# Performance work log

Measured on AMD Instinct MI355X. Metric: run time of the kernel, lower is better.

## Reference

```python
import jax, jax.numpy as jnp
import numpy as np

B, N, D, O, H, R = 32, 1024, 1024, 1024, 512, 64
TOPK = 4
MAX_GAIN = 0.1
SCALE = 1.0
LN_EPS = 1e-5


def _dct_basis(dim, num_bases):
    pos = np.arange(dim, dtype=np.float64)[None, :]
    modes = np.arange(num_bases, dtype=np.float64)[:, None]
    basis = np.cos(np.pi / dim * (pos + 0.5) * modes)
    basis[0] = basis[0] / np.sqrt(2.0)
    basis = basis * np.sqrt(2.0 / dim)
    return jnp.asarray(basis, jnp.float32)


def setup_inputs() -> dict:
    key = jax.random.key(0)
    ks = jax.random.split(key, 16)
    s = 0.02
    return {
        'x': jax.random.normal(ks[0], (B, N, D), jnp.float32),
        'context': jax.random.normal(ks[1], (B, H), jnp.float32),
        'input_basis': _dct_basis(D, R),                       # [R, D] (buffer)
        'output_basis': s * jax.random.normal(ks[2], (R, O), jnp.float32),
        'ln_gamma': jnp.ones((D,), jnp.float32),
        'ln_beta': jnp.zeros((D,), jnp.float32),
        'w1': s * jax.random.normal(ks[3], (D, H), jnp.float32),
        'b1': jnp.zeros((H,), jnp.float32),
        'w2': s * jax.random.normal(ks[4], (H, H), jnp.float32),
        'b2': jnp.zeros((H,), jnp.float32),
        'wg': s * jax.random.normal(ks[5], (H, R * R), jnp.float32),
        'bg': jnp.zeros((R * R,), jnp.float32),
        'wl': s * jax.random.normal(ks[6], (H, R * R), jnp.float32),
        'bl': jnp.zeros((R * R,), jnp.float32),
        'wm': s * jax.random.normal(ks[7], (2 * H, R), jnp.float32),
        'bm': 1.5 * jnp.ones((R,), jnp.float32),
        'wgain': s * jax.random.normal(ks[8], (2 * H, R), jnp.float32),
        'bgain': jnp.zeros((R,), jnp.float32),
        'wgate': s * jax.random.normal(ks[9], (2 * H, 1), jnp.float32),
        'bgate': -1.0 * jnp.ones((1,), jnp.float32),
        'wa': s * jax.random.normal(ks[10], (2 * H, 1), jnp.float32),
        'ba': -1.0 * jnp.ones((1,), jnp.float32),
        'wb': s * jax.random.normal(ks[11], (2 * H, 1), jnp.float32),
        'bb': jnp.zeros((1,), jnp.float32),
    }


def _detail_summary(x, topk):
    # x: [B, N, D] with token 0 = CLS; pick topk highest-variance patch tokens
    pt = x[:, 1:]                                   # [B, N-1, D]
    pm = jnp.mean(pt, axis=1, keepdims=True)
    scores = jnp.mean((pt - pm) ** 2, axis=-1)      # [B, N-1]
    _, idx = jax.lax.top_k(scores, topk)            # [B, k]
    gathered = jnp.take_along_axis(pt, idx[:, :, None], axis=1)  # [B, k, D]
    return jnp.mean(gathered, axis=1)               # [B, D]


def _skew(a):
    return 0.5 * (a - jnp.swapaxes(a, -1, -2))


def reference(x, context, input_basis, output_basis, ln_gamma, ln_beta,
              w1, b1, w2, b2, wg, bg, wl, bl, wm, bm,
              wgain, bgain, wgate, bgate, wa, ba, wb, bb):
    b = x.shape[0]
    r = input_basis.shape[0]

    detail = _detail_summary(x, TOPK)               # [B, D]
    mu = jnp.mean(detail, axis=-1, keepdims=True)
    var = jnp.var(detail, axis=-1, keepdims=True)
    h = (detail - mu) * jax.lax.rsqrt(var + LN_EPS) * ln_gamma + ln_beta
    h = jax.nn.gelu(h @ w1 + b1, approximate=False)
    local_context = h @ w2 + b2                     # [B, H]
    fused = jnp.concatenate([context, local_context], axis=-1)  # [B, 2H]

    global_skew = _skew((context @ wg + bg).reshape(b, r, r))
    local_skew = _skew((local_context @ wl + bl).reshape(b, r, r))
    mode_mask = jax.nn.sigmoid(fused @ wm + bm)     # [B, R]
    # diag(m) @ A @ diag(m) == m_i * A_ij * m_j
    mg = mode_mask[:, :, None] * global_skew * mode_mask[:, None, :]
    ml = mode_mask[:, :, None] * local_skew * mode_mask[:, None, :]
    comm = ml @ mg - mg @ ml                        # [B, R, R]

    alpha = SCALE * 0.5 * jax.nn.sigmoid(fused @ wa + ba)   # [B, 1]
    beta = SCALE * 0.25 * jnp.tanh(fused @ wb + bb)         # [B, 1]
    omega = alpha[:, :, None] * 0.5 * (mg + ml) + beta[:, :, None] * (comm / 12.0)

    q = jax.vmap(jax.scipy.linalg.expm)(omega)              # [B, R, R]
    gains = 1.0 + MAX_GAIN * jnp.tanh(fused @ wgain + bgain)  # [B, R]
    operator = q * gains[:, None, :]                        # q @ diag(gains)

    proj = jnp.einsum('bnd,rd->bnr', x, input_basis)        # [B, N, R]
    gate = SCALE * jax.nn.sigmoid(fused @ wgate + bgate)    # [B, 1]
    transformed = jnp.einsum('bnr,brk->bnk', proj, operator)
    delta = gate[:, None, :] * (transformed - proj)         # [B, N, R]
    out = jnp.einsum('bnr,ro->bno', delta, output_basis)    # [B, N, O]
    return out
```

## Files before the change

### kernel.cpp

```cpp
#include <hip/hip_runtime.h>
#include <math.h>

#define NB 32
#define NN 1024
#define ND 1024
#define NO 1024
#define NH 512
#define NR 64

#define OFF_PM     0u
#define OFF_PMSQ   32768u
#define OFF_ROWSQ  32800u
#define OFF_G      65568u
#define OFF_H0     98336u
#define OFF_H1     131104u
#define OFF_LOCAL  147488u
#define OFF_P1     163872u
#define OFF_P2     294944u
#define OFF_PG     360480u
#define OFF_PL     884768u
#define OFF_AG     1409056u
#define OFF_AL     1540128u
#define OFF_MASK   1671200u
#define OFF_GAINS  1673248u
#define OFF_SCAL   1675296u
#define OFF_MFIN   1675424u
#define OFF_C      1806496u
#define OFF_PROJ   3903648u

__global__ __launch_bounds__(256) void k0_colsum(const float* __restrict__ x, float* __restrict__ part){
  int tid = threadIdx.x;
  int nseg = blockIdx.x, b = blockIdx.y;
  int d4 = tid*4;
  const float* xp = x + (size_t)b*NN*ND + d4;
  int nstart = nseg*64; if(nseg==0) nstart = 1;
  int nend = nseg*64 + 64;
  float sx=0.f, sy=0.f, sz=0.f, sw=0.f;
  #pragma unroll 4
  for(int n=nstart; n<nend; n++){
    float4 v = *(const float4*)&xp[(size_t)n*ND];
    sx+=v.x; sy+=v.y; sz+=v.z; sw+=v.w;
  }
  *(float4*)&part[(size_t)(b*16+nseg)*1024 + d4] = make_float4(sx,sy,sz,sw);
}

__global__ __launch_bounds__(256) void k1_pmreduce(const float* __restrict__ part, float* __restrict__ pm, float* __restrict__ pmsq){
  __shared__ float red[256];
  int b = blockIdx.x, tid = threadIdx.x;
  float acc = 0.f;
  #pragma unroll
  for(int i=0;i<4;i++){
    int d = i*256 + tid;
    float s = 0.f;
    #pragma unroll
    for(int ks=0;ks<16;ks++) s += part[(size_t)(b*16+ks)*1024 + d];
    float p = s * (1.0f/1023.0f);
    pm[b*1024+d] = p;
    acc += p*p;
  }
  red[tid] = acc; __syncthreads();
  for(int o=128;o>0;o>>=1){ if(tid<o) red[tid]+=red[tid+o]; __syncthreads(); }
  if(tid==0) pmsq[b] = red[0]*(1.0f/1024.0f);
}

__global__ __launch_bounds__(256) void k2_proj(const float* __restrict__ x, const float* __restrict__ basis,
    const float* __restrict__ pm, float* __restrict__ proj, float* __restrict__ rowsq, float* __restrict__ G){
  __shared__ __align__(16) float xs[64][68];
  __shared__ __align__(16) float bs[64][68];
  int tid = threadIdx.x;
  int row0 = blockIdx.x*64;
  int b = row0 >> 10;
  int lrow = tid>>4, lkv = tid&15;
  int rg = tid>>4, cg = tid&15;
  float acc[4][4];
  #pragma unroll
  for(int i_=0;i_<4;i_++){ acc[i_][0]=0.f; acc[i_][1]=0.f; acc[i_][2]=0.f; acc[i_][3]=0.f; }
  float sq[4]={0.f,0.f,0.f,0.f}, gp[4]={0.f,0.f,0.f,0.f};
  for(int kc=0;kc<16;kc++){
    int k0 = kc*64;
    float4 p4 = *(const float4*)&pm[(size_t)b*ND + k0 + lkv*4];
    #pragma unroll
    for(int i=0;i<4;i++){
      int r = lrow + 16*i;
      float4 v = *(const float4*)&x[((size_t)(row0+r))*ND + k0 + lkv*4];
      xs[lkv*4+0][r]=v.x; xs[lkv*4+1][r]=v.y; xs[lkv*4+2][r]=v.z; xs[lkv*4+3][r]=v.w;
      sq[i] += v.x*v.x + v.y*v.y + v.z*v.z + v.w*v.w;
      gp[i] += v.x*p4.x + v.y*p4.y + v.z*p4.z + v.w*p4.w;
      float4 u = *(const float4*)&basis[((size_t)r)*ND + k0 + lkv*4];
      bs[lkv*4+0][r]=u.x; bs[lkv*4+1][r]=u.y; bs[lkv*4+2][r]=u.z; bs[lkv*4+3][r]=u.w;
    }
    __syncthreads();
    #pragma unroll 8
    for(int kk=0;kk<64;kk++){
      float4 a = *(const float4*)&xs[kk][rg*4];
      float4 bb= *(const float4*)&bs[kk][cg*4];
      float ar[4]={a.x,a.y,a.z,a.w};
      float br[4]={bb.x,bb.y,bb.z,bb.w};
      #pragma unroll
      for(int i_=0;i_<4;i_++){
        #pragma unroll
        for(int j_=0;j_<4;j_++) acc[i_][j_] += ar[i_]*br[j_];
      }
    }
    __syncthreads();
  }
  #pragma unroll
  for(int i_=0;i_<4;i_++){
    float4 v = make_float4(acc[i_][0],acc[i_][1],acc[i_][2],acc[i_][3]);
    *(float4*)&proj[((size_t)(row0 + rg*4 + i_))*NR + cg*4] = v;
  }
  __syncthreads();
  #pragma unroll
  for(int i=0;i<4;i++){ int r = lrow+16*i; xs[r][lkv]=sq[i]; bs[r][lkv]=gp[i]; }
  __syncthreads();
  if(tid<64){
    float s=0.f, g=0.f;
    #pragma unroll
    for(int c=0;c<16;c++){ s+=xs[tid][c]; g+=bs[tid][c]; }
    rowsq[row0+tid]=s; G[row0+tid]=g;
  }
}

__global__ __launch_bounds__(256) void k3_detail(const float* __restrict__ x, const float* __restrict__ rowsq,
    const float* __restrict__ G, const float* __restrict__ pmsq,
    const float* __restrict__ gamma_, const float* __restrict__ beta_, float* __restrict__ h0){
  __shared__ float sc[1024];
  __shared__ float rv[256];
  __shared__ int ri[256];
  __shared__ int topi[4];
  __shared__ float mred[256];
  int b = blockIdx.x, tid = threadIdx.x;
  float ps = pmsq[b];
  const float invD = 1.0f/1024.0f;
  for(int n=tid;n<1024;n+=256)
    sc[n] = (n==0) ? -INFINITY : (rowsq[b*1024+n] - 2.0f*G[b*1024+n])*invD + ps;
  __syncthreads();
  for(int t=0;t<4;t++){
    float bv = -INFINITY; int bi = 0x7fffffff;
    for(int n=tid;n<1024;n+=256){
      float v = sc[n];
      if(v>bv || (v==bv && n<bi)){ bv=v; bi=n; }
    }
    rv[tid]=bv; ri[tid]=bi;
    __syncthreads();
    for(int o=128;o>0;o>>=1){
      if(tid<o){
        float v=rv[tid+o]; int ii=ri[tid+o];
        if(v>rv[tid] || (v==rv[tid] && ii<ri[tid])){ rv[tid]=v; ri[tid]=ii; }
      }
      __syncthreads();
    }
    if(tid==0){ topi[t]=ri[0]; sc[ri[0]] = -INFINITY; }
    __syncthreads();
  }
  int i0=topi[0], i1=topi[1], i2=topi[2], i3=topi[3];
  float dv[4]; float dsum=0.f;
  #pragma unroll
  for(int jj=0;jj<4;jj++){
    int d = tid + jj*256;
    float v = 0.25f*(x[((size_t)(b*NN+i0))*ND+d] + x[((size_t)(b*NN+i1))*ND+d]
                   + x[((size_t)(b*NN+i2))*ND+d] + x[((size_t)(b*NN+i3))*ND+d]);
    dv[jj]=v; dsum+=v;
  }
  mred[tid]=dsum; __syncthreads();
  for(int o=128;o>0;o>>=1){ if(tid<o) mred[tid]+=mred[tid+o]; __syncthreads(); }
  float mu = mred[0]*invD;
  __syncthreads();
  float vs=0.f;
  #pragma unroll
  for(int jj=0;jj<4;jj++){ float t2=dv[jj]-mu; vs+=t2*t2; }
  mred[tid]=vs; __syncthreads();
  for(int o=128;o>0;o>>=1){ if(tid<o) mred[tid]+=mred[tid+o]; __syncthreads(); }
  float var = mred[0]*invD;
  float rstd = rsqrtf(var + 1e-5f);
  #pragma unroll
  for(int jj=0;jj<4;jj++){
    int d = tid + jj*256;
    h0[b*1024+d] = (dv[jj]-mu)*rstd*gamma_[d] + beta_[d];
  }
}

__global__ __launch_bounds__(256) void gemm32_partial(const float* __restrict__ V, const float* __restrict__ W,
      float* __restrict__ part, int Kd, int Ncols){
  __shared__ __align__(16) float Vs[128][36];
  int col = blockIdx.x*256 + threadIdx.x;
  int k0 = blockIdx.y*128;
  for(int i=threadIdx.x; i<4096; i+=256){ int r=i>>7, k=i&127; Vs[k][r] = V[(size_t)r*Kd + k0 + k]; }
  __syncthreads();
  float acc[32];
  #pragma unroll
  for(int r=0;r<32;r++) acc[r]=0.f;
  #pragma unroll 4
  for(int k=0;k<128;k++){
    float wv = W[(size_t)(k0+k)*Ncols + col];
    #pragma unroll
    for(int r4=0;r4<8;r4++){
      float4 v = *(const float4*)&Vs[k][r4*4];
      acc[r4*4+0]+=v.x*wv; acc[r4*4+1]+=v.y*wv; acc[r4*4+2]+=v.z*wv; acc[r4*4+3]+=v.w*wv;
    }
  }
  #pragma unroll
  for(int r=0;r<32;r++) part[((size_t)(blockIdx.y*32 + r))*Ncols + col] = acc[r];
}

__global__ __launch_bounds__(256) void k_red_gelu(const float* __restrict__ part, const float* __restrict__ b1, float* __restrict__ h1){
  int id = blockIdx.x*256 + threadIdx.x;
  int b_ = id >> 9, j = id & 511;
  float s = b1[j];
  #pragma unroll
  for(int ks=0;ks<8;ks++) s += part[(size_t)(ks*32+b_)*512 + j];
  h1[id] = 0.5f*s*(1.0f + erff(s*0.70710678118654752440f));
}
__global__ __launch_bounds__(256) void k_red_local(const float* __restrict__ part, const float* __restrict__ b2, float* __restrict__ lcl){
  int id = blockIdx.x*256 + threadIdx.x;
  int b_ = id >> 9, j = id & 511;
  float s = b2[j];
  #pragma unroll
  for(int ks=0;ks<4;ks++) s += part[(size_t)(ks*32+b_)*512 + j];
  lcl[id] = s;
}
__global__ __launch_bounds__(256) void k_red_gl(const float* __restrict__ pg, const float* __restrict__ pl,
    const float* __restrict__ bg, const float* __restrict__ bl, float* __restrict__ Ag, float* __restrict__ Al){
  int id = blockIdx.x*256 + threadIdx.x;
  int c = id & 4095;
  int b_ = id >> 12;
  float sg = bg[c], sl = bl[c];
  #pragma unroll
  for(int ks=0;ks<4;ks++){
    sg += pg[(size_t)(ks*32 + b_)*4096 + c];
    sl += pl[(size_t)(ks*32 + b_)*4096 + c];
  }
  Ag[id] = sg; Al[id] = sl;
}

__global__ __launch_bounds__(1024) void k_heads(const float* __restrict__ context, const float* __restrict__ lcl,
    const float* __restrict__ wm, const float* __restrict__ bm,
    const float* __restrict__ wgain, const float* __restrict__ bgain,
    const float* __restrict__ wgate, const float* __restrict__ bgate,
    const float* __restrict__ wa, const float* __restrict__ ba,
    const float* __restrict__ wb, const float* __restrict__ bb,
    float* __restrict__ mask, float* __restrict__ gains, float* __restrict__ scal){
  __shared__ float fs[1024];
  __shared__ float redm[16][64];
  __shared__ float redg[16][64];
  __shared__ float wra[16], wrb[16], wrg[16];
  int b = blockIdx.x, tid = threadIdx.x;
  fs[tid] = (tid < 512) ? context[b*512 + tid] : lcl[b*512 + tid - 512];
  __syncthreads();
  int j = tid & 63, kq = tid >> 6;
  const float* wmp = wm    + (size_t)(kq*64)*64 + j;
  const float* wgp = wgain + (size_t)(kq*64)*64 + j;
  float am = 0.f, ag = 0.f;
  #pragma unroll 8
  for(int k=0;k<64;k++){
    float f = fs[kq*64 + k];
    am += f * wmp[k*64];
    ag += f * wgp[k*64];
  }
  redm[kq][j] = am; redg[kq][j] = ag;
  float f = fs[tid];
  float pa = f*wa[tid], pb = f*wb[tid], pg = f*wgate[tid];
  #pragma unroll
  for(int o=32;o>0;o>>=1){
    pa += __shfl_down(pa, o);
    pb += __shfl_down(pb, o);
    pg += __shfl_down(pg, o);
  }
  if(j == 0){ wra[kq]=pa; wrb[kq]=pb; wrg[kq]=pg; }
  __syncthreads();
  for(int o=8;o>0;o>>=1){
    if(kq < o){ redm[kq][j] += redm[kq+o][j]; redg[kq][j] += redg[kq+o][j]; }
    __syncthreads();
  }
  if(tid < 64){
    float m = redm[0][tid] + bm[tid];
    mask[b*64+tid] = 1.0f/(1.0f+expf(-m));
    float g = redg[0][tid] + bgain[tid];
    gains[b*64+tid] = 1.0f + 0.1f*tanhf(g);
  }
  if(tid == 0){
    float sa=0.f, sb=0.f, sg=0.f;
    #pragma unroll
    for(int i=0;i<16;i++){ sa+=wra[i]; sb+=wrb[i]; sg+=wrg[i]; }
    scal[b*4+0] = 0.5f/(1.0f+expf(-(sa+ba[0])));
    scal[b*4+1] = 0.25f*tanhf(sb+bb[0]);
    scal[b*4+2] = 1.0f/(1.0f+expf(-(sg+bgate[0])));
  }
}

__global__ __launch_bounds__(1024) void k7_expm(const float* __restrict__ Ag, const float* __restrict__ Al,
    const float* __restrict__ mask, const float* __restrict__ gains, const float* __restrict__ scal,
    float* __restrict__ Mfin){
  __shared__ __align__(16) float B0s[64][66];
  __shared__ __align__(16) float B1s[64][66];
  __shared__ __align__(16) float B2s[64][66];
  __shared__ float msks[64];
  __shared__ float colsum[64];
  __shared__ int ssh;
  int b = blockIdx.x, tid = threadIdx.x;
  int ig = tid>>5, jg = tid&31;
  int i0 = ig*2, j0 = jg*2;
  if(tid<64) msks[tid] = mask[b*64+tid];
  __syncthreads();
  float alpha = scal[b*4+0], bta = scal[b*4+1], gate = scal[b*4+2];
  const float* ag = Ag + b*4096;
  const float* al = Al + b*4096;
  #pragma unroll
  for(int di=0;di<2;di++){
    #pragma unroll
    for(int dj=0;dj<2;dj++){
      int i=i0+di, jx=j0+dj;
      float mm_ = msks[i]*msks[jx]*0.5f;
      B0s[i][jx] = mm_*(ag[i*64+jx]-ag[jx*64+i]);
      B1s[i][jx] = mm_*(al[i*64+jx]-al[jx*64+i]);
    }
  }
  __syncthreads();
  {
    float c00=0.f,c01=0.f,c10=0.f,c11=0.f;
    #pragma unroll 4
    for(int k=0;k<64;k++){
      float a0=B1s[i0][k], a1=B1s[i0+1][k];
      float m0=B0s[i0][k], m1=B0s[i0+1][k];
      float2 u = *(const float2*)&B0s[k][j0];
      float2 w = *(const float2*)&B1s[k][j0];
      c00 += a0*u.x - m0*w.x;  c01 += a0*u.y - m0*w.y;
      c10 += a1*u.x - m1*w.x;  c11 += a1*u.y - m1*w.y;
    }
    B2s[i0][j0]=c00; B2s[i0][j0+1]=c01; B2s[i0+1][j0]=c10; B2s[i0+1][j0+1]=c11;
  }
  __syncthreads();
  const float bc = bta*(1.0f/12.0f);
  #pragma unroll
  for(int di=0;di<2;di++){
    #pragma unroll
    for(int dj=0;dj<2;dj++){
      int i=i0+di, jx=j0+dj;
      B0s[i][jx] = alpha*0.5f*(B0s[i][jx]+B1s[i][jx]) + bc*B2s[i][jx];
    }
  }
  __syncthreads();
  if(tid<64){
    float s=0.f;
    for(int i=0;i<64;i++) s += fabsf(B0s[i][tid]);
    colsum[tid]=s;
  }
  __syncthreads();
  if(tid==0){
    float m=0.f;
    for(int jx=0;jx<64;jx++) m = fmaxf(m, colsum[jx]);
    int s=0;
    while(m>0.5f && s<30){ m*=0.5f; s++; }
    ssh = s;
  }
  __syncthreads();
  int sh = ssh;
  float scl = ldexpf(1.0f, -sh);
  #pragma unroll
  for(int di=0;di<2;di++){
    #pragma unroll
    for(int dj=0;dj<2;dj++){ int i=i0+di,jx=j0+dj; B0s[i][jx]*=scl; }
  }
  __syncthreads();
  #pragma unroll
  for(int di=0;di<2;di++){
    #pragma unroll
    for(int dj=0;dj<2;dj++){
      int i=i0+di, jx=j0+dj;
      B1s[i][jx] = ((i==jx)?1.0f:0.0f) + B0s[i][jx]*0.125f;
    }
  }
  __syncthreads();
  for(int kk=7;kk>=1;kk--){
    float c00=0.f,c01=0.f,c10=0.f,c11=0.f;
    #pragma unroll 4
    for(int k=0;k<64;k++){
      float a0=B0s[i0][k], a1=B0s[i0+1][k];
      float2 u = *(const float2*)&B1s[k][j0];
      c00+=a0*u.x; c01+=a0*u.y; c10+=a1*u.x; c11+=a1*u.y;
    }
    B2s[i0][j0]=c00; B2s[i0][j0+1]=c01; B2s[i0+1][j0]=c10; B2s[i0+1][j0+1]=c11;
    __syncthreads();
    float inv = 1.0f/(float)kk;
    #pragma unroll
    for(int di=0;di<2;di++){
      #pragma unroll
      for(int dj=0;dj<2;dj++){
        int i=i0+di, jx=j0+dj;
        B1s[i][jx] = ((i==jx)?1.0f:0.0f) + B2s[i][jx]*inv;
      }
    }
    __syncthreads();
  }
  float (*Q)[66] = B1s; float (*T)[66] = B2s;
  for(int t=0;t<sh;t++){
    float c00=0.f,c01=0.f,c10=0.f,c11=0.f;
    #pragma unroll 4
    for(int k=0;k<64;k++){
      float a0=Q[i0][k], a1=Q[i0+1][k];
      float2 u = *(const float2*)&Q[k][j0];
      c00+=a0*u.x; c01+=a0*u.y; c10+=a1*u.x; c11+=a1*u.y;
    }
    T[i0][j0]=c00; T[i0][j0+1]=c01; T[i0+1][j0]=c10; T[i0+1][j0+1]=c11;
    __syncthreads();
    float (*tmp)[66]=Q; Q=T; T=tmp;
  }
  float g0 = gains[b*64+j0], g1 = gains[b*64+j0+1];
  float* mf = Mfin + b*4096;
  #pragma unroll
  for(int di=0;di<2;di++){
    int i=i0+di;
    float2 v;
    v.x = gate*(Q[i][j0]*g0   - ((i==j0)?1.0f:0.0f));
    v.y = gate*(Q[i][j0+1]*g1 - ((i==j0+1)?1.0f:0.0f));
    *(float2*)&mf[i*64+j0] = v;
  }
}

__global__ __launch_bounds__(256) void k8_cmat(const float* __restrict__ Mfin, const float* __restrict__ ob, float* __restrict__ C){
  __shared__ __align__(16) float MT[64][68];
  int b = blockIdx.y; int o0 = blockIdx.x*128;
  int tid = threadIdx.x;
  for(int idx=tid; idx<4096; idx+=256){ int i=idx>>6, k=idx&63; MT[k][i] = Mfin[b*4096+idx]; }
  __syncthreads();
  int cg = tid&31, rg = tid>>5;
  float acc[8][4];
  #pragma unroll
  for(int r=0;r<8;r++){ acc[r][0]=0.f; acc[r][1]=0.f; acc[r][2]=0.f; acc[r][3]=0.f; }
  for(int k=0;k<64;k++){
    float4 bv = *(const float4*)&ob[(size_t)k*NO + o0 + cg*4];
    float4 a0 = *(const float4*)&MT[k][rg*8];
    float4 a1 = *(const float4*)&MT[k][rg*8+4];
    float arr[8]={a0.x,a0.y,a0.z,a0.w,a1.x,a1.y,a1.z,a1.w};
    #pragma unroll
    for(int r=0;r<8;r++){
      acc[r][0]+=arr[r]*bv.x; acc[r][1]+=arr[r]*bv.y; acc[r][2]+=arr[r]*bv.z; acc[r][3]+=arr[r]*bv.w;
    }
  }
  #pragma unroll
  for(int r=0;r<8;r++){
    *(float4*)&C[((size_t)(b*64 + rg*8+r))*NO + o0 + cg*4] = make_float4(acc[r][0],acc[r][1],acc[r][2],acc[r][3]);
  }
}

__global__ __launch_bounds__(256) void k9_out(const float* __restrict__ proj, const float* __restrict__ C, float* __restrict__ out){
  __shared__ __align__(16) float PT[64][132];
  __shared__ __align__(16) float CS[64][68];
  int b = blockIdx.z; int row0 = blockIdx.y*128; int o0 = blockIdx.x*64;
  int tid = threadIdx.x;
  #pragma unroll
  for(int i=0;i<8;i++){
    int f = tid + 256*i; int r = f>>4; int kv = f&15;
    float4 v = *(const float4*)&proj[((size_t)(b*NN + row0 + r))*NR + kv*4];
    PT[kv*4+0][r]=v.x; PT[kv*4+1][r]=v.y; PT[kv*4+2][r]=v.z; PT[kv*4+3][r]=v.w;
  }
  #pragma unroll
  for(int i=0;i<4;i++){
    int f = tid + 256*i; int k = f>>4; int kv = f&15;
    *(float4*)&CS[k][kv*4] = *(const float4*)&C[((size_t)(b*NR + k))*NO + o0 + kv*4];
  }
  __syncthreads();
  int rg = tid>>4, cg = tid&15;
  float acc[8][4];
  #pragma unroll
  for(int r=0;r<8;r++){ acc[r][0]=0.f; acc[r][1]=0.f; acc[r][2]=0.f; acc[r][3]=0.f; }
  #pragma unroll 8
  for(int k=0;k<64;k++){
    float4 bv = *(const float4*)&CS[k][cg*4];
    float4 a0 = *(const float4*)&PT[k][rg*8];
    float4 a1 = *(const float4*)&PT[k][rg*8+4];
    float arr[8]={a0.x,a0.y,a0.z,a0.w,a1.x,a1.y,a1.z,a1.w};
    #pragma unroll
    for(int r=0;r<8;r++){
      acc[r][0]+=arr[r]*bv.x; acc[r][1]+=arr[r]*bv.y; acc[r][2]+=arr[r]*bv.z; acc[r][3]+=arr[r]*bv.w;
    }
  }
  #pragma unroll
  for(int r=0;r<8;r++){
    *(float4*)&out[((size_t)(b*NN + row0 + rg*8 + r))*NO + o0 + cg*4] =
        make_float4(acc[r][0],acc[r][1],acc[r][2],acc[r][3]);
  }
}

extern "C" void kernel_launch(void* const* d_in, const int* in_sizes, int n_in,
                              void* d_out, int out_size, void* d_ws, size_t ws_size,
                              hipStream_t stream) {
  (void)in_sizes; (void)n_in; (void)out_size; (void)ws_size;
  const float* x       = (const float*)d_in[0];
  const float* context = (const float*)d_in[1];
  const float* ibasis  = (const float*)d_in[2];
  const float* obasis  = (const float*)d_in[3];
  const float* lng     = (const float*)d_in[4];
  const float* lnb     = (const float*)d_in[5];
  const float* w1      = (const float*)d_in[6];
  const float* b1      = (const float*)d_in[7];
  const float* w2      = (const float*)d_in[8];
  const float* b2      = (const float*)d_in[9];
  const float* wg      = (const float*)d_in[10];
  const float* bg      = (const float*)d_in[11];
  const float* wl      = (const float*)d_in[12];
  const float* bl      = (const float*)d_in[13];
  const float* wm      = (const float*)d_in[14];
  const float* bm      = (const float*)d_in[15];
  const float* wgain   = (const float*)d_in[16];
  const float* bgain   = (const float*)d_in[17];
  const float* wgate   = (const float*)d_in[18];
  const float* bgate   = (const float*)d_in[19];
  const float* wa      = (const float*)d_in[20];
  const float* ba      = (const float*)d_in[21];
  const float* wb      = (const float*)d_in[22];
  const float* bb      = (const float*)d_in[23];
  float* out = (float*)d_out;
  float* ws  = (float*)d_ws;

  float* pm    = ws + OFF_PM;
  float* pmsq  = ws + OFF_PMSQ;
  float* rowsq = ws + OFF_ROWSQ;
  float* G     = ws + OFF_G;
  float* h0    = ws + OFF_H0;
  float* h1    = ws + OFF_H1;
  float* lcl   = ws + OFF_LOCAL;
  float* p1    = ws + OFF_P1;
  float* p2    = ws + OFF_P2;
  float* pg_   = ws + OFF_PG;
  float* part  = ws + OFF_PG;
  float* pl_   = ws + OFF_PL;
  float* Ag    = ws + OFF_AG;
  float* Al    = ws + OFF_AL;
  float* mask  = ws + OFF_MASK;
  float* gains = ws + OFF_GAINS;
  float* scal  = ws + OFF_SCAL;
  float* Mfin  = ws + OFF_MFIN;
  float* Cb    = ws + OFF_C;
  float* proj  = ws + OFF_PROJ;

  k0_colsum<<<dim3(16,NB),256,0,stream>>>(x, part);
  k1_pmreduce<<<NB,256,0,stream>>>(part, pm, pmsq);
  k2_proj<<<512,256,0,stream>>>(x, ibasis, pm, proj, rowsq, G);
  k3_detail<<<NB,256,0,stream>>>(x, rowsq, G, pmsq, lng, lnb, h0);
  gemm32_partial<<<dim3(2,8),256,0,stream>>>(h0, w1, p1, 1024, 512);
  k_red_gelu<<<64,256,0,stream>>>(p1, b1, h1);
  gemm32_partial<<<dim3(2,4),256,0,stream>>>(h1, w2, p2, 512, 512);
  k_red_local<<<64,256,0,stream>>>(p2, b2, lcl);
  gemm32_partial<<<dim3(16,4),256,0,stream>>>(context, wg, pg_, 512, 4096);
  gemm32_partial<<<dim3(16,4),256,0,stream>>>(lcl, wl, pl_, 512, 4096);
  k_red_gl<<<512,256,0,stream>>>(pg_, pl_, bg, bl, Ag, Al);
  k_heads<<<NB,1024,0,stream>>>(context, lcl, wm, bm, wgain, bgain, wgate, bgate, wa, ba, wb, bb, mask, gains, scal);
  k7_expm<<<NB,1024,0,stream>>>(Ag, Al, mask, gains, scal, Mfin);
  k8_cmat<<<dim3(8,NB),256,0,stream>>>(Mfin, obasis, Cb);
  k9_out<<<dim3(16,8,NB),256,0,stream>>>(proj, Cb, out);
}
```

Before: 612.7 us.

## Rewrite projection as LDS-free register GEMM over a transposed basis

```diff
diff --git a/kernel.cpp b/kernel.cpp
--- a/kernel.cpp
+++ b/kernel.cpp
@@ -27,11 +27,34 @@
 #define OFF_MFIN   1675424u
 #define OFF_C      1806496u
 #define OFF_PROJ   3903648u
-
-__global__ __launch_bounds__(256) void k0_colsum(const float* __restrict__ x, float* __restrict__ part){
+#define OFF_BT     6000800u
+
+__global__ __launch_bounds__(256) void kT_basis(const float* __restrict__ basis, float* __restrict__ basisT){
+  __shared__ float s[64][65];
+  int d0 = blockIdx.x*64;
+  int tid = threadIdx.x;
+  #pragma unroll
+  for(int i=0;i<16;i++){
+    int idx = i*256 + tid;
+    int r = idx>>6, dl = idx&63;
+    s[r][dl] = basis[(size_t)r*ND + d0 + dl];
+  }
+  __syncthreads();
+  #pragma unroll
+  for(int i=0;i<16;i++){
+    int idx = i*256 + tid;
+    int dl = idx>>6, r = idx&63;
+    basisT[(size_t)(d0+dl)*64 + r] = s[r][dl];
+  }
+}
+
+__global__ __launch_bounds__(256) void k0_colsum(const float* __restrict__ x, float* __restrict__ part,
+    float* __restrict__ rowsq){
+  __shared__ float red[4][64];
   int tid = threadIdx.x;
   int nseg = blockIdx.x, b = blockIdx.y;
   int d4 = tid*4;
+  int lane = tid & 63, wv = tid >> 6;
   const float* xp = x + (size_t)b*NN*ND + d4;
   int nstart = nseg*64; if(nseg==0) nstart = 1;
   int nend = nseg*64 + 64;
@@ -40,8 +63,16 @@
   for(int n=nstart; n<nend; n++){
     float4 v = *(const float4*)&xp[(size_t)n*ND];
     sx+=v.x; sy+=v.y; sz+=v.z; sw+=v.w;
+    float s = v.x*v.x + v.y*v.y + v.z*v.z + v.w*v.w;
+    #pragma unroll
+    for(int o=32;o>0;o>>=1) s += __shfl_down(s, o);
+    if(lane==0) red[wv][n - nseg*64] = s;
   }
   *(float4*)&part[(size_t)(b*16+nseg)*1024 + d4] = make_float4(sx,sy,sz,sw);
+  __syncthreads();
+  if(tid < 64 && !(nseg==0 && tid==0)){
+    rowsq[b*1024 + nseg*64 + tid] = red[0][tid]+red[1][tid]+red[2][tid]+red[3][tid];
+  }
 }
 
 __global__ __launch_bounds__(256) void k1_pmreduce(const float* __restrict__ part, float* __restrict__ pm, float* __restrict__ pmsq){
@@ -63,62 +94,46 @@
   if(tid==0) pmsq[b] = red[0]*(1.0f/1024.0f);
 }
 
-__global__ __launch_bounds__(256) void k2_proj(const float* __restrict__ x, const float* __restrict__ basis,
-    const float* __restrict__ pm, float* __restrict__ proj, float* __restrict__ rowsq, float* __restrict__ G){
-  __shared__ __align__(16) float xs[64][68];
-  __shared__ __align__(16) float bs[64][68];
+__global__ __launch_bounds__(256) void k2_proj(const float* __restrict__ x, const float* __restrict__ bT,
+    const float* __restrict__ pm, float* __restrict__ proj, float* __restrict__ G){
   int tid = threadIdx.x;
-  int row0 = blockIdx.x*64;
+  int row0 = blockIdx.x*32;
   int b = row0 >> 10;
-  int lrow = tid>>4, lkv = tid&15;
   int rg = tid>>4, cg = tid&15;
-  float acc[4][4];
-  #pragma unroll
-  for(int i_=0;i_<4;i_++){ acc[i_][0]=0.f; acc[i_][1]=0.f; acc[i_][2]=0.f; acc[i_][3]=0.f; }
-  float sq[4]={0.f,0.f,0.f,0.f}, gp[4]={0.f,0.f,0.f,0.f};
-  for(int kc=0;kc<16;kc++){
-    int k0 = kc*64;
-    float4 p4 = *(const float4*)&pm[(size_t)b*ND + k0 + lkv*4];
-    #pragma unroll
-    for(int i=0;i<4;i++){
-      int r = lrow + 16*i;
-      float4 v = *(const float4*)&x[((size_t)(row0+r))*ND + k0 + lkv*4];
-      xs[lkv*4+0][r]=v.x; xs[lkv*4+1][r]=v.y; xs[lkv*4+2][r]=v.z; xs[lkv*4+3][r]=v.w;
-      sq[i] += v.x*v.x + v.y*v.y + v.z*v.z + v.w*v.w;
-      gp[i] += v.x*p4.x + v.y*p4.y + v.z*p4.z + v.w*p4.w;
-      float4 u = *(const float4*)&basis[((size_t)r)*ND + k0 + lkv*4];
-      bs[lkv*4+0][r]=u.x; bs[lkv*4+1][r]=u.y; bs[lkv*4+2][r]=u.z; bs[lkv*4+3][r]=u.w;
-    }
-    __syncthreads();
-    #pragma unroll 8
-    for(int kk=0;kk<64;kk++){
-      float4 a = *(const float4*)&xs[kk][rg*4];
-      float4 bb= *(const float4*)&bs[kk][cg*4];
-      float ar[4]={a.x,a.y,a.z,a.w};
-      float br[4]={bb.x,bb.y,bb.z,bb.w};
-      #pragma unroll
-      for(int i_=0;i_<4;i_++){
-        #pragma unroll
-        for(int j_=0;j_<4;j_++) acc[i_][j_] += ar[i_]*br[j_];
-      }
-    }
-    __syncthreads();
-  }
-  #pragma unroll
-  for(int i_=0;i_<4;i_++){
-    float4 v = make_float4(acc[i_][0],acc[i_][1],acc[i_][2],acc[i_][3]);
-    *(float4*)&proj[((size_t)(row0 + rg*4 + i_))*NR + cg*4] = v;
-  }
-  __syncthreads();
-  #pragma unroll
-  for(int i=0;i<4;i++){ int r = lrow+16*i; xs[r][lkv]=sq[i]; bs[r][lkv]=gp[i]; }
-  __syncthreads();
-  if(tid<64){
-    float s=0.f, g=0.f;
-    #pragma unroll
-    for(int c=0;c<16;c++){ s+=xs[tid][c]; g+=bs[tid][c]; }
-    rowsq[row0+tid]=s; G[row0+tid]=g;
-  }
+  int r0 = row0 + rg*2;
+  const float* xr0 = x + (size_t)r0*ND;
+  const float* xr1 = xr0 + ND;
+  const float* pmb = pm + (size_t)b*ND;
+  const float* bc  = bT + cg*4;
+  float4 acc0 = make_float4(0.f,0.f,0.f,0.f);
+  float4 acc1 = make_float4(0.f,0.f,0.f,0.f);
+  float g0 = 0.f, g1 = 0.f;
+  #pragma unroll 2
+  for(int k=0;k<ND;k+=4){
+    float4 a0 = *(const float4*)&xr0[k];
+    float4 a1 = *(const float4*)&xr1[k];
+    float4 p  = *(const float4*)&pmb[k];
+    float4 b0 = *(const float4*)&bc[(size_t)(k+0)*64];
+    float4 b1 = *(const float4*)&bc[(size_t)(k+1)*64];
+    float4 b2 = *(const float4*)&bc[(size_t)(k+2)*64];
+    float4 b3 = *(const float4*)&bc[(size_t)(k+3)*64];
+    float ar0[4]={a0.x,a0.y,a0.z,a0.w};
+    float ar1[4]={a1.x,a1.y,a1.z,a1.w};
+    float pr[4]={p.x,p.y,p.z,p.w};
+    float4 bb[4]={b0,b1,b2,b3};
+    #pragma unroll
+    for(int j=0;j<4;j++){
+      acc0.x += ar0[j]*bb[j].x; acc0.y += ar0[j]*bb[j].y;
+      acc0.z += ar0[j]*bb[j].z; acc0.w += ar0[j]*bb[j].w;
+      acc1.x += ar1[j]*bb[j].x; acc1.y += ar1[j]*bb[j].y;
+      acc1.z += ar1[j]*bb[j].z; acc1.w += ar1[j]*bb[j].w;
+      g0 += ar0[j]*pr[j];
+      g1 += ar1[j]*pr[j];
+    }
+  }
+  *(float4*)&proj[(size_t)r0*NR + cg*4]     = acc0;
+  *(float4*)&proj[(size_t)(r0+1)*NR + cg*4] = acc1;
+  if(cg==0){ G[r0] = g0; G[r0+1] = g1; }
 }
 
 __global__ __launch_bounds__(256) void k3_detail(const float* __restrict__ x, const float* __restrict__ rowsq,
@@ -533,10 +548,12 @@
   float* Mfin  = ws + OFF_MFIN;
   float* Cb    = ws + OFF_C;
   float* proj  = ws + OFF_PROJ;
-
-  k0_colsum<<<dim3(16,NB),256,0,stream>>>(x, part);
+  float* bT    = ws + OFF_BT;
+
+  kT_basis<<<16,256,0,stream>>>(ibasis, bT);
+  k0_colsum<<<dim3(16,NB),256,0,stream>>>(x, part, rowsq);
   k1_pmreduce<<<NB,256,0,stream>>>(part, pm, pmsq);
-  k2_proj<<<512,256,0,stream>>>(x, ibasis, pm, proj, rowsq, G);
+  k2_proj<<<1024,256,0,stream>>>(x, bT, pm, proj, G);
   k3_detail<<<NB,256,0,stream>>>(x, rowsq, G, pmsq, lng, lnb, h0);
   gemm32_partial<<<dim3(2,8),256,0,stream>>>(h0, w1, p1, 1024, 512);
   k_red_gelu<<<64,256,0,stream>>>(p1, b1, h1);
```

Measured after the change: 719.7 us. 1.17x slower.

## Split projection GEMM along K, pretranspose basis, swizzle LDS, move row norms to colsum

Applied to the files above, without the earlier changes.

```diff
diff --git a/kernel.cpp b/kernel.cpp
--- a/kernel.cpp
+++ b/kernel.cpp
@@ -27,11 +27,34 @@
 #define OFF_MFIN   1675424u
 #define OFF_C      1806496u
 #define OFF_PROJ   3903648u
-
-__global__ __launch_bounds__(256) void k0_colsum(const float* __restrict__ x, float* __restrict__ part){
+#define OFF_BT     6000800u
+
+__global__ __launch_bounds__(256) void kT_basis(const float* __restrict__ basis, float* __restrict__ basisT){
+  __shared__ float s[64][65];
+  int d0 = blockIdx.x*64;
+  int tid = threadIdx.x;
+  #pragma unroll
+  for(int i=0;i<16;i++){
+    int idx = i*256 + tid;
+    int r = idx>>6, dl = idx&63;
+    s[r][dl] = basis[(size_t)r*ND + d0 + dl];
+  }
+  __syncthreads();
+  #pragma unroll
+  for(int i=0;i<16;i++){
+    int idx = i*256 + tid;
+    int dl = idx>>6, r = idx&63;
+    basisT[(size_t)(d0+dl)*64 + r] = s[r][dl];
+  }
+}
+
+__global__ __launch_bounds__(256) void k0_colsum(const float* __restrict__ x, float* __restrict__ part,
+    float* __restrict__ rowsq){
+  __shared__ float red[4][64];
   int tid = threadIdx.x;
   int nseg = blockIdx.x, b = blockIdx.y;
   int d4 = tid*4;
+  int lane = tid & 63, wv = tid >> 6;
   const float* xp = x + (size_t)b*NN*ND + d4;
   int nstart = nseg*64; if(nseg==0) nstart = 1;
   int nend = nseg*64 + 64;
@@ -40,8 +63,16 @@
   for(int n=nstart; n<nend; n++){
     float4 v = *(const float4*)&xp[(size_t)n*ND];
     sx+=v.x; sy+=v.y; sz+=v.z; sw+=v.w;
+    float s = v.x*v.x + v.y*v.y + v.z*v.z + v.w*v.w;
+    #pragma unroll
+    for(int o=32;o>0;o>>=1) s += __shfl_down(s, o);
+    if(lane==0) red[wv][n - nseg*64] = s;
   }
   *(float4*)&part[(size_t)(b*16+nseg)*1024 + d4] = make_float4(sx,sy,sz,sw);
+  __syncthreads();
+  if(tid < 64 && !(nseg==0 && tid==0)){
+    rowsq[b*1024 + nseg*64 + tid] = red[0][tid]+red[1][tid]+red[2][tid]+red[3][tid];
+  }
 }
 
 __global__ __launch_bounds__(256) void k1_pmreduce(const float* __restrict__ part, float* __restrict__ pm, float* __restrict__ pmsq){
@@ -63,36 +94,44 @@
   if(tid==0) pmsq[b] = red[0]*(1.0f/1024.0f);
 }
 
-__global__ __launch_bounds__(256) void k2_proj(const float* __restrict__ x, const float* __restrict__ basis,
-    const float* __restrict__ pm, float* __restrict__ proj, float* __restrict__ rowsq, float* __restrict__ G){
+__global__ __launch_bounds__(256) void k2_proj(const float* __restrict__ x, const float* __restrict__ bT,
+    const float* __restrict__ pm, float* __restrict__ proj, float* __restrict__ projp,
+    float* __restrict__ G, float* __restrict__ Gp){
   __shared__ __align__(16) float xs[64][68];
   __shared__ __align__(16) float bs[64][68];
   int tid = threadIdx.x;
   int row0 = blockIdx.x*64;
   int b = row0 >> 10;
+  int kh = blockIdx.y;
+  int kbase = kh*512;
   int lrow = tid>>4, lkv = tid&15;
   int rg = tid>>4, cg = tid&15;
   float acc[4][4];
   #pragma unroll
   for(int i_=0;i_<4;i_++){ acc[i_][0]=0.f; acc[i_][1]=0.f; acc[i_][2]=0.f; acc[i_][3]=0.f; }
-  float sq[4]={0.f,0.f,0.f,0.f}, gp[4]={0.f,0.f,0.f,0.f};
-  for(int kc=0;kc<16;kc++){
-    int k0 = kc*64;
+  float gp[4]={0.f,0.f,0.f,0.f};
+  int sw = ((lkv>>1)&3)<<2;
+  for(int kc=0;kc<8;kc++){
+    int k0 = kbase + kc*64;
     float4 p4 = *(const float4*)&pm[(size_t)b*ND + k0 + lkv*4];
     #pragma unroll
     for(int i=0;i<4;i++){
       int r = lrow + 16*i;
       float4 v = *(const float4*)&x[((size_t)(row0+r))*ND + k0 + lkv*4];
-      xs[lkv*4+0][r]=v.x; xs[lkv*4+1][r]=v.y; xs[lkv*4+2][r]=v.z; xs[lkv*4+3][r]=v.w;
-      sq[i] += v.x*v.x + v.y*v.y + v.z*v.z + v.w*v.w;
+      int rs = r ^ sw;
+      xs[lkv*4+0][rs]=v.x; xs[lkv*4+1][rs]=v.y; xs[lkv*4+2][rs]=v.z; xs[lkv*4+3][rs]=v.w;
       gp[i] += v.x*p4.x + v.y*p4.y + v.z*p4.z + v.w*p4.w;
-      float4 u = *(const float4*)&basis[((size_t)r)*ND + k0 + lkv*4];
-      bs[lkv*4+0][r]=u.x; bs[lkv*4+1][r]=u.y; bs[lkv*4+2][r]=u.z; bs[lkv*4+3][r]=u.w;
+    }
+    #pragma unroll
+    for(int i=0;i<4;i++){
+      int idx = tid + 256*i;
+      int kk = idx>>4, kv = idx&15;
+      *(float4*)&bs[kk][kv*4] = *(const float4*)&bT[((size_t)(k0+kk))*64 + kv*4];
     }
     __syncthreads();
     #pragma unroll 8
     for(int kk=0;kk<64;kk++){
-      float4 a = *(const float4*)&xs[kk][rg*4];
+      float4 a = *(const float4*)&xs[kk][ (rg ^ ((kk>>3)&3)) << 2 ];
       float4 bb= *(const float4*)&bs[kk][cg*4];
       float ar[4]={a.x,a.y,a.z,a.w};
       float br[4]={bb.x,bb.y,bb.z,bb.w};
@@ -104,25 +143,33 @@
     }
     __syncthreads();
   }
+  float* dst = kh ? projp : proj;
   #pragma unroll
   for(int i_=0;i_<4;i_++){
     float4 v = make_float4(acc[i_][0],acc[i_][1],acc[i_][2],acc[i_][3]);
-    *(float4*)&proj[((size_t)(row0 + rg*4 + i_))*NR + cg*4] = v;
-  }
-  __syncthreads();
-  #pragma unroll
-  for(int i=0;i<4;i++){ int r = lrow+16*i; xs[r][lkv]=sq[i]; bs[r][lkv]=gp[i]; }
+    *(float4*)&dst[((size_t)(row0 + rg*4 + i_))*NR + cg*4] = v;
+  }
+  #pragma unroll
+  for(int i=0;i<4;i++){ int r = lrow+16*i; bs[r][lkv]=gp[i]; }
   __syncthreads();
   if(tid<64){
-    float s=0.f, g=0.f;
-    #pragma unroll
-    for(int c=0;c<16;c++){ s+=xs[tid][c]; g+=bs[tid][c]; }
-    rowsq[row0+tid]=s; G[row0+tid]=g;
-  }
+    float g=0.f;
+    #pragma unroll
+    for(int c=0;c<16;c++) g += bs[tid][c];
+    if(kh) Gp[row0+tid] = g; else G[row0+tid] = g;
+  }
+}
+
+__global__ __launch_bounds__(256) void k2_red(float* __restrict__ proj, const float* __restrict__ projp){
+  int id = blockIdx.x*256 + threadIdx.x;
+  float4 a = *(const float4*)&proj[(size_t)id*4];
+  float4 p = *(const float4*)&projp[(size_t)id*4];
+  a.x+=p.x; a.y+=p.y; a.z+=p.z; a.w+=p.w;
+  *(float4*)&proj[(size_t)id*4] = a;
 }
 
 __global__ __launch_bounds__(256) void k3_detail(const float* __restrict__ x, const float* __restrict__ rowsq,
-    const float* __restrict__ G, const float* __restrict__ pmsq,
+    const float* __restrict__ G, const float* __restrict__ Gp, const float* __restrict__ pmsq,
     const float* __restrict__ gamma_, const float* __restrict__ beta_, float* __restrict__ h0){
   __shared__ float sc[1024];
   __shared__ float rv[256];
@@ -133,7 +180,7 @@
   float ps = pmsq[b];
   const float invD = 1.0f/1024.0f;
   for(int n=tid;n<1024;n+=256)
-    sc[n] = (n==0) ? -INFINITY : (rowsq[b*1024+n] - 2.0f*G[b*1024+n])*invD + ps;
+    sc[n] = (n==0) ? -INFINITY : (rowsq[b*1024+n] - 2.0f*(G[b*1024+n]+Gp[b*1024+n]))*invD + ps;
   __syncthreads();
   for(int t=0;t<4;t++){
     float bv = -INFINITY; int bi = 0x7fffffff;
@@ -524,6 +571,7 @@
   float* p2    = ws + OFF_P2;
   float* pg_   = ws + OFF_PG;
   float* part  = ws + OFF_PG;
+  float* Gp    = ws + OFF_PG;
   float* pl_   = ws + OFF_PL;
   float* Ag    = ws + OFF_AG;
   float* Al    = ws + OFF_AL;
@@ -532,12 +580,16 @@
   float* scal  = ws + OFF_SCAL;
   float* Mfin  = ws + OFF_MFIN;
   float* Cb    = ws + OFF_C;
+  float* projp = ws + OFF_C;
   float* proj  = ws + OFF_PROJ;
-
-  k0_colsum<<<dim3(16,NB),256,0,stream>>>(x, part);
+  float* bT    = ws + OFF_BT;
+
+  kT_basis<<<16,256,0,stream>>>(ibasis, bT);
+  k0_colsum<<<dim3(16,NB),256,0,stream>>>(x, part, rowsq);
   k1_pmreduce<<<NB,256,0,stream>>>(part, pm, pmsq);
-  k2_proj<<<512,256,0,stream>>>(x, ibasis, pm, proj, rowsq, G);
-  k3_detail<<<NB,256,0,stream>>>(x, rowsq, G, pmsq, lng, lnb, h0);
+  k2_proj<<<dim3(512,2),256,0,stream>>>(x, bT, pm, proj, projp, G, Gp);
+  k2_red<<<2048,256,0,stream>>>(proj, projp);
+  k3_detail<<<NB,256,0,stream>>>(x, rowsq, G, Gp, pmsq, lng, lnb, h0);
   gemm32_partial<<<dim3(2,8),256,0,stream>>>(h0, w1, p1, 1024, 512);
   k_red_gelu<<<64,256,0,stream>>>(p1, b1, h1);
   gemm32_partial<<<dim3(2,4),256,0,stream>>>(h1, w2, p2, 512, 512);
```

Result: no change. 612.2 us (-0.1%).
